# Kernel optimization log

Measured on AMD Instinct MI355X. Metric: run time of the kernel, lower is better.

The kernel has to match this reference:

```python
import jax, jax.numpy as jnp
import numpy as np

WIN = 9  # 9x9 local attention window

def conv2d(x, w, b=None, pad=1):
    # x: [B,C,H,W], w: [O,I,kh,kw]
    y = jax.lax.conv_general_dilated(x, w, (1, 1), [(pad, pad), (pad, pad)],
                                     dimension_numbers=('NCHW', 'OIHW', 'NCHW'))
    if b is not None:
        y = y + b[None, :, None, None]
    return y

def leaky(x):
    return jax.nn.leaky_relu(x, 0.2)

def local_similar(q, k):
    # TorchLocalAttention.f_similar: per-pixel dot(q[i,j], k[i+di-4, j+dj-4]) with zero pad,
    # kernel positions row-major (di*9+dj) -> output [B, 81, H, W]
    b, c, h, w = q.shape
    r = WIN // 2
    kp = jnp.pad(k, ((0, 0), (0, 0), (r, r), (r, r)))
    sims = []
    for di in range(WIN):
        for dj in range(WIN):
            sims.append(jnp.einsum('bchw,bchw->bhw', q, kp[:, :, di:di + h, dj:dj + w]))
    return jnp.stack(sims, axis=1)

def srp_forward(old, new, wq, bq, wk, bk, wv, bv, wo1, bo1, res_w1, res_w2, wo2, bo2):
    x = jnp.concatenate((old, new), axis=1)  # [B, C, H, W]
    att = local_similar(conv2d(x, wq, bq), conv2d(x, wk, bk))  # [B, 81, H, W]
    v = conv2d(att, wv, bv)  # [B, C, H, W]
    y = conv2d(x * v, wo1, bo1)
    n_res = res_w1.shape[0]
    for i in range(n_res):  # EBlock: ResBlocks (convs bias=False)
        h1 = leaky(conv2d(y, res_w1[i]))
        y = y + conv2d(h1, res_w2[i])
    y = conv2d(y, wo2, bo2)
    return y + x

def setup_inputs() -> dict:
    key = jax.random.key(0)
    B, Cn, Co, H, W = 4, 32, 32, 256, 256
    C = Cn + Co
    NRES = 8
    ks = jax.random.split(key, 16)
    s = 0.05
    inp = {
        'old': jax.random.normal(ks[0], (B, Co, H, W), jnp.float32),
        'new': jax.random.normal(ks[1], (B, Cn, H, W), jnp.float32),
        'wq': jax.random.normal(ks[2], (C, C, 3, 3), jnp.float32) * s,
        'bq': jax.random.normal(ks[3], (C,), jnp.float32) * s,
        'wk': jax.random.normal(ks[4], (C, C, 3, 3), jnp.float32) * s,
        'bk': jax.random.normal(ks[5], (C,), jnp.float32) * s,
        'wv': jax.random.normal(ks[6], (C, 81, 3, 3), jnp.float32) * s,
        'bv': jax.random.normal(ks[7], (C,), jnp.float32) * s,
        'wo1': jax.random.normal(ks[8], (C, C, 3, 3), jnp.float32) * s,
        'bo1': jax.random.normal(ks[9], (C,), jnp.float32) * s,
        'res_w1': jax.random.normal(ks[10], (NRES, C, C, 3, 3), jnp.float32) * s,
        'res_w2': jax.random.normal(ks[11], (NRES, C, C, 3, 3), jnp.float32) * s,
        'wo2': jax.random.normal(ks[12], (C, C, 3, 3), jnp.float32) * s,
        'bo2': jax.random.normal(ks[13], (C,), jnp.float32) * s,
    }
    return inp

def reference(old, new, wq, bq, wk, bk, wv, bv, wo1, bo1, res_w1, res_w2, wo2, bo2):
    return srp_forward(old, new, wq, bq, wk, bk, wv, bv, wo1, bo1, res_w1, res_w2, wo2, bo2)
```

## Files before the change

### kernel.cpp

```cpp
#include <hip/hip_runtime.h>
#include <hip/hip_bf16.h>


#define HH 256
#define WW 256
#define PLANE 65536

typedef _Float16 f16x8 __attribute__((ext_vector_type(8)));
typedef float    f32x4 __attribute__((ext_vector_type(4)));
typedef _Float16 h2    __attribute__((ext_vector_type(2)));

__device__ __forceinline__ unsigned short f2h(float f) {
    _Float16 h = (_Float16)f;
    return __builtin_bit_cast(unsigned short, h);
}
__device__ __forceinline__ float h2f(unsigned short u) {
    return (float)__builtin_bit_cast(_Float16, u);
}
__device__ __forceinline__ unsigned pack2h(float a, float b) {
    return (unsigned)f2h(a) | ((unsigned)f2h(b) << 16);
}
__device__ __forceinline__ float dot2h(unsigned a, unsigned b, float c) {
#if __has_builtin(__builtin_amdgcn_fdot2)
    return __builtin_amdgcn_fdot2(__builtin_bit_cast(h2, a),
                                  __builtin_bit_cast(h2, b), c, false);
#else
    h2 av = __builtin_bit_cast(h2, a), bv = __builtin_bit_cast(h2, b);
    return fmaf((float)av.x, (float)bv.x, fmaf((float)av.y, (float)bv.y, c));
#endif
}

__device__ __forceinline__ void gl16(const unsigned short* g, unsigned short* l) {
    __builtin_amdgcn_global_load_lds(
        (const __attribute__((address_space(1))) unsigned int*)(g),
        (__attribute__((address_space(3))) unsigned int*)(l),
        16, 0, 0);
}

template <int CIN, bool BIAS, bool LEAKY, bool ADDF, bool ADDX, bool MULX, bool OUTF, bool OUTB>
__global__ __launch_bounds__(256, 2) void conv_mfma(
    const unsigned short* __restrict__ in_pc,
    const unsigned short* __restrict__ wb,
    const float* __restrict__ bias,
    const unsigned short* __restrict__ addh,
    const unsigned short* __restrict__ xh,
    float* __restrict__ outf,
    unsigned short* __restrict__ outb)
{
    __shared__ unsigned short smem[28800];
    unsigned short* lds_in = smem;
    unsigned short* lds_w  = smem + 10368;

    const int tid = threadIdx.x;
    const int w   = tid >> 6;
    const int ln  = tid & 63;
    const int m   = ln & 15;
    const int q   = ln >> 4;
    const int b   = blockIdx.z;
    const int tx0 = blockIdx.x * 16, ty0 = blockIdx.y * 16;
    const size_t pixb = (size_t)b * PLANE;
    const bool interior = (blockIdx.x >= 1) && (blockIdx.x <= 14) &&
                          (blockIdx.y >= 1) && (blockIdx.y <= 14);

    f32x4 acc[4][4];
#pragma unroll
    for (int g = 0; g < 4; ++g)
#pragma unroll
        for (int p = 0; p < 4; ++p) acc[g][p] = (f32x4)0.f;

    for (int c2 = 0; c2 < CIN / 32; ++c2) {
        __syncthreads();
        if (interior) {
            const unsigned short* inb =
                in_pc + (pixb + (size_t)(ty0 - 1) * 256 + (tx0 - 1)) * CIN + c2 * 32;
#pragma unroll
            for (int it = 0; it < 5; ++it) {
                int u = it * 256 + tid;
                int pix = u >> 2, ps = u & 3;
                int part = ps ^ (pix & 3);
                int hy = pix / 18, hx = pix - hy * 18;
                gl16(inb + ((size_t)hy * 256 + hx) * CIN + part * 8,
                     &lds_in[(it * 256 + (tid & 192)) * 8]);
            }
            if (tid < 16) {
                int u = 1280 + tid;
                int pix = u >> 2, ps = u & 3;
                int part = ps ^ (pix & 3);
                int hy = pix / 18, hx = pix - hy * 18;
                gl16(inb + ((size_t)hy * 256 + hx) * CIN + part * 8,
                     &lds_in[1280 * 8]);
            }
        } else {
            for (int u = tid; u < 1296; u += 256) {
                int pix = u >> 2, part = u & 3;
                int hy = pix / 18, hx = pix - hy * 18;
                int gy = ty0 + hy - 1, gx = tx0 + hx - 1;
                uint4 val = make_uint4(0u, 0u, 0u, 0u);
                if ((unsigned)gy < 256u && (unsigned)gx < 256u)
                    val = *reinterpret_cast<const uint4*>(
                        in_pc + ((pixb + (size_t)gy * 256 + gx) * CIN + c2 * 32 + part * 8));
                *reinterpret_cast<uint4*>(&lds_in[pix * 32 + ((part ^ (pix & 3)) * 8)]) = val;
            }
        }
        {
            const int oc = tid >> 2, ps = tid & 3;
            const int part = ps ^ (oc & 3);
            const unsigned short* wsrc = wb + (size_t)oc * CIN + c2 * 32 + part * 8;
#pragma unroll
            for (int t = 0; t < 9; ++t)
                gl16(wsrc + (size_t)t * 64 * CIN,
                     &lds_w[t * 2048 + (tid & 192) * 8]);
        }
        __syncthreads();

#pragma unroll
        for (int t = 0; t < 9; ++t) {
            const int dy = t / 3, dx = t - dy * 3;
            f16x8 av[4], bv[4];
#pragma unroll
            for (int g = 0; g < 4; ++g) {
                int oc = g * 16 + m;
                av[g] = *reinterpret_cast<const f16x8*>(
                    &lds_w[t * 2048 + oc * 32 + ((q ^ (oc & 3)) * 8)]);
            }
#pragma unroll
            for (int p = 0; p < 4; ++p) {
                int hp = (w * 4 + p + dy) * 18 + m + dx;
                bv[p] = *reinterpret_cast<const f16x8*>(
                    &lds_in[hp * 32 + ((q ^ (hp & 3)) * 8)]);
            }
#pragma unroll
            for (int g = 0; g < 4; ++g)
#pragma unroll
                for (int p = 0; p < 4; ++p)
                    acc[g][p] = __builtin_amdgcn_mfma_f32_16x16x32_f16(
                        av[g], bv[p], acc[g][p], 0, 0, 0);
        }
    }

    const int colx = tx0 + m;
    float4 bvec[4];
    if (BIAS) {
#pragma unroll
        for (int g = 0; g < 4; ++g)
            bvec[g] = *reinterpret_cast<const float4*>(bias + g * 16 + q * 4);
    }
    if (OUTB) __syncthreads();

#pragma unroll
    for (int g = 0; g < 4; ++g) {
#pragma unroll
        for (int p = 0; p < 4; ++p) {
            const int prow = w * 4 + p;
            const int gy   = ty0 + prow;
            const size_t pixg = pixb + (size_t)gy * 256 + colx;
            const int oc0 = g * 16 + q * 4;
            ushort4 a4, x4;
            if (ADDF) a4 = *reinterpret_cast<const ushort4*>(addh + pixg * 64 + oc0);
            if (ADDX || MULX) x4 = *reinterpret_cast<const ushort4*>(xh + pixg * 64 + oc0);
            float vals[4];
#pragma unroll
            for (int r = 0; r < 4; ++r) {
                float v = acc[g][p][r];
                if (BIAS) v += reinterpret_cast<const float*>(&bvec[g])[r];
                if (LEAKY) v = (v >= 0.f) ? v : 0.2f * v;
                if (ADDF) v += h2f(reinterpret_cast<const unsigned short*>(&a4)[r]);
                if (ADDX) v += h2f(reinterpret_cast<const unsigned short*>(&x4)[r]);
                if (MULX) v *= h2f(reinterpret_cast<const unsigned short*>(&x4)[r]);
                if (OUTF)
                    outf[((size_t)(b * 64 + oc0 + r)) * PLANE + (size_t)gy * 256 + colx] = v;
                vals[r] = v;
            }
            if (OUTB) {
                ushort4 pk;
                pk.x = f2h(vals[0]); pk.y = f2h(vals[1]);
                pk.z = f2h(vals[2]); pk.w = f2h(vals[3]);
                int pix   = prow * 16 + m;
                int part8 = g * 4 + q;
                int p16   = (part8 >> 1) ^ (pix & 7);
                *reinterpret_cast<ushort4*>(&smem[pix * 64 + p16 * 8 + (part8 & 1) * 4]) = pk;
            }
        }
    }
    if (OUTB) {
        __syncthreads();
        for (int u = tid; u < 2048; u += 256) {
            int pix = u >> 3, p16 = u & 7;
            uint4 val = *reinterpret_cast<const uint4*>(
                &smem[pix * 64 + ((p16 ^ (pix & 7)) * 8)]);
            int gy = ty0 + (pix >> 4), gx = tx0 + (pix & 15);
            *reinterpret_cast<uint4*>(
                &outb[(pixb + (size_t)gy * 256 + gx) * 64 + p16 * 8]) = val;
        }
    }
}

__global__ __launch_bounds__(256)
void local_sim(
    const unsigned short* __restrict__ qh, const unsigned short* __restrict__ kh,
    unsigned short* __restrict__ att)
{
    __shared__ unsigned short lds_k[576 * 64];

    const int tid = threadIdx.x;
    const int tx = tid & 15, ty = tid >> 4;
    const int bx = blockIdx.x * 16, by = blockIdx.y * 16;
    const int b  = blockIdx.z;
    const size_t pixb = (size_t)b * PLANE;
    const bool interior = (blockIdx.x >= 1) && (blockIdx.x <= 14) &&
                          (blockIdx.y >= 1) && (blockIdx.y <= 14);

    if (interior) {
        const unsigned short* kb =
            kh + (pixb + (size_t)(by - 4) * 256 + (bx - 4)) * 64;
#pragma unroll
        for (int it = 0; it < 18; ++it) {
            int u = it * 256 + tid;
            int pix = u >> 3, sl = u & 7;
            int part = sl ^ ((pix ^ (pix >> 3)) & 7);
            int hy = pix / 24, hx = pix - hy * 24;
            gl16(kb + ((size_t)hy * 256 + hx) * 64 + part * 8,
                 &lds_k[(it * 256 + (tid & 192)) * 8]);
        }
    } else {
        for (int u = tid; u < 4608; u += 256) {
            int pix = u >> 3, part = u & 7;
            int hy = pix / 24, hx = pix - hy * 24;
            int gy = by + hy - 4, gx = bx + hx - 4;
            uint4 val = make_uint4(0u, 0u, 0u, 0u);
            if ((unsigned)gy < 256u && (unsigned)gx < 256u)
                val = *reinterpret_cast<const uint4*>(
                    kh + ((pixb + (size_t)gy * 256 + gx) * 64 + part * 8));
            int sl = part ^ ((pix ^ (pix >> 3)) & 7);
            *reinterpret_cast<uint4*>(&lds_k[pix * 64 + sl * 8]) = val;
        }
    }
    __syncthreads();

    const unsigned short* qbase = qh + (pixb + (size_t)(by + ty) * 256 + bx + tx) * 64;
    unsigned short* op = att + (pixb + (size_t)(by + ty) * 256 + bx + tx) * 96;

    uint4 qv[8];
#pragma unroll
    for (int j = 0; j < 8; ++j)
        qv[j] = *reinterpret_cast<const uint4*>(qbase + j * 8);

#pragma unroll
    for (int g = 0; g < 3; ++g) {
        float acc[27];
#pragma unroll
        for (int i = 0; i < 27; ++i) acc[i] = 0.f;

#pragma unroll
        for (int dil = 0; dil < 3; ++dil) {
            const int hrow = (ty + g * 3 + dil) * 24 + tx;
#pragma unroll
            for (int dj = 0; dj < 9; ++dj) {
                const int hp = hrow + dj;
                const int gs = (hp ^ (hp >> 3)) & 7;
                float s = acc[dil * 9 + dj];
#pragma unroll
                for (int part = 0; part < 8; ++part) {
                    const uint4 kv = *reinterpret_cast<const uint4*>(
                        &lds_k[hp * 64 + ((part ^ gs) * 8)]);
                    s = dot2h(qv[part].x, kv.x, s);
                    s = dot2h(qv[part].y, kv.y, s);
                    s = dot2h(qv[part].z, kv.z, s);
                    s = dot2h(qv[part].w, kv.w, s);
                }
                acc[dil * 9 + dj] = s;
            }
        }

        unsigned short* o = op + g * 27;
        if (g == 0) {
            uint4 A = {pack2h(acc[0], acc[1]),  pack2h(acc[2], acc[3]),
                       pack2h(acc[4], acc[5]),  pack2h(acc[6], acc[7])};
            uint4 B = {pack2h(acc[8], acc[9]),  pack2h(acc[10], acc[11]),
                       pack2h(acc[12], acc[13]), pack2h(acc[14], acc[15])};
            uint2 C = {pack2h(acc[16], acc[17]), pack2h(acc[18], acc[19])};
            uint2 D = {pack2h(acc[20], acc[21]), pack2h(acc[22], acc[23])};
            *reinterpret_cast<uint4*>(o)      = A;
            *reinterpret_cast<uint4*>(o + 8)  = B;
            *reinterpret_cast<uint2*>(o + 16) = C;
            *reinterpret_cast<uint2*>(o + 20) = D;
            *reinterpret_cast<unsigned*>(o + 24) = pack2h(acc[24], acc[25]);
            o[26] = f2h(acc[26]);
        } else if (g == 1) {
            o[0] = f2h(acc[0]);
            *reinterpret_cast<unsigned*>(o + 1) = pack2h(acc[1], acc[2]);
            *reinterpret_cast<unsigned*>(o + 3) = pack2h(acc[3], acc[4]);
            uint4 A = {pack2h(acc[5], acc[6]),   pack2h(acc[7], acc[8]),
                       pack2h(acc[9], acc[10]),  pack2h(acc[11], acc[12])};
            uint4 B = {pack2h(acc[13], acc[14]), pack2h(acc[15], acc[16]),
                       pack2h(acc[17], acc[18]), pack2h(acc[19], acc[20])};
            *reinterpret_cast<uint4*>(o + 5)  = A;
            *reinterpret_cast<uint4*>(o + 13) = B;
            uint2 C = {pack2h(acc[21], acc[22]), pack2h(acc[23], acc[24])};
            *reinterpret_cast<uint2*>(o + 21) = C;
            *reinterpret_cast<unsigned*>(o + 25) = pack2h(acc[25], acc[26]);
        } else {
            *reinterpret_cast<unsigned*>(o) = pack2h(acc[0], acc[1]);
            uint4 A = {pack2h(acc[2], acc[3]),   pack2h(acc[4], acc[5]),
                       pack2h(acc[6], acc[7]),   pack2h(acc[8], acc[9])};
            uint4 B = {pack2h(acc[10], acc[11]), pack2h(acc[12], acc[13]),
                       pack2h(acc[14], acc[15]), pack2h(acc[16], acc[17])};
            *reinterpret_cast<uint4*>(o + 2)  = A;
            *reinterpret_cast<uint4*>(o + 10) = B;
            uint2 C = {pack2h(acc[18], acc[19]), pack2h(acc[20], acc[21])};
            *reinterpret_cast<uint2*>(o + 18) = C;
            *reinterpret_cast<unsigned*>(o + 22) = pack2h(acc[22], acc[23]);
            *reinterpret_cast<unsigned*>(o + 24) = pack2h(acc[24], acc[25]);
            o[26] = f2h(acc[26]);
        }
    }

    op[81] = 0;
    *reinterpret_cast<unsigned*>(op + 82) = 0u;
    uint2 z2 = {0u, 0u};
    uint4 z4 = {0u, 0u, 0u, 0u};
    *reinterpret_cast<uint2*>(op + 84) = z2;
    *reinterpret_cast<uint4*>(op + 88) = z4;
}

__global__ __launch_bounds__(256) void pack_x(
    const float* __restrict__ old_, const float* __restrict__ new_,
    unsigned short* __restrict__ xb)
{
    __shared__ unsigned short lds[256 * 64];
    const int tid = threadIdx.x;
    const int b = blockIdx.y;
    const size_t pixbase = (size_t)blockIdx.x * 256;
#pragma unroll
    for (int cg = 0; cg < 8; ++cg) {
        unsigned pk[4];
#pragma unroll
        for (int h = 0; h < 4; ++h) {
            int c0 = cg * 8 + h * 2;
            const float* s0 = (c0 < 32) ? old_ : new_;
            const float* s1 = ((c0 + 1) < 32) ? old_ : new_;
            float f0 = s0[((size_t)b * 32 + (c0 & 31)) * PLANE + pixbase + tid];
            float f1 = s1[((size_t)b * 32 + ((c0 + 1) & 31)) * PLANE + pixbase + tid];
            pk[h] = pack2h(f0, f1);
        }
        int p16 = cg ^ (tid & 7);
        uint4 v; v.x = pk[0]; v.y = pk[1]; v.z = pk[2]; v.w = pk[3];
        *reinterpret_cast<uint4*>(&lds[tid * 64 + p16 * 8]) = v;
    }
    __syncthreads();
    for (int r = 0; r < 8; ++r) {
        int u = r * 256 + tid;
        int pix = u >> 3, p16 = u & 7;
        uint4 v = *reinterpret_cast<const uint4*>(&lds[pix * 64 + ((p16 ^ (pix & 7)) * 8)]);
        *reinterpret_cast<uint4*>(
            &xb[((size_t)b * PLANE + pixbase + pix) * 64 + p16 * 8]) = v;
    }
}

__global__ void prep_wstd(const float* __restrict__ wq, const float* __restrict__ wk,
                          const float* __restrict__ wo1, const float* __restrict__ wo2,
                          const float* __restrict__ rw1, const float* __restrict__ rw2,
                          unsigned short* __restrict__ wstd)
{
    const int c = blockIdx.y;
    const float* src;
    if (c == 0) src = wq;
    else if (c == 1) src = wk;
    else if (c == 2) src = wo1;
    else if (c == 3) src = wo2;
    else if (c < 12) src = rw1 + (size_t)(c - 4) * 36864;
    else src = rw2 + (size_t)(c - 12) * 36864;
    int idx = blockIdx.x * 256 + threadIdx.x;
    int o = idx >> 6, i = idx & 63;
    const float* s = src + (size_t)(o * 64 + i) * 9;
    unsigned short* d = wstd + (size_t)c * 36864 + (size_t)o * 64 + i;
#pragma unroll
    for (int t = 0; t < 9; ++t) d[(size_t)t * 4096] = f2h(s[t]);
}

__global__ void prep_wv(const float* __restrict__ wv, unsigned short* __restrict__ wv96)
{
    int idx = blockIdx.x * 256 + threadIdx.x;
    int o = idx / 96, i = idx - o * 96;
    unsigned short* d = wv96 + (size_t)o * 96 + i;
    if (i < 81) {
        const float* s = wv + (size_t)(o * 81 + i) * 9;
#pragma unroll
        for (int t = 0; t < 9; ++t) d[(size_t)t * 6144] = f2h(s[t]);
    } else {
#pragma unroll
        for (int t = 0; t < 9; ++t) d[(size_t)t * 6144] = 0;
    }
}

extern "C" void kernel_launch(void* const* d_in, const int* in_sizes, int n_in,
                              void* d_out, int out_size, void* d_ws, size_t ws_size,
                              hipStream_t stream)
{
    const float* old_ = (const float*)d_in[0];
    const float* new_ = (const float*)d_in[1];
    const float* wq  = (const float*)d_in[2];  const float* bq  = (const float*)d_in[3];
    const float* wk  = (const float*)d_in[4];  const float* bk  = (const float*)d_in[5];
    const float* wv  = (const float*)d_in[6];  const float* bv  = (const float*)d_in[7];
    const float* wo1 = (const float*)d_in[8];  const float* bo1 = (const float*)d_in[9];
    const float* rw1 = (const float*)d_in[10]; const float* rw2 = (const float*)d_in[11];
    const float* wo2 = (const float*)d_in[12]; const float* bo2 = (const float*)d_in[13];
    float* out = (float*)d_out;

    char* ws = (char*)d_ws;
    unsigned short* X   = (unsigned short*)(ws);
    unsigned short* P1  = (unsigned short*)(ws + 33554432ull);
    unsigned short* P2  = (unsigned short*)(ws + 67108864ull);
    unsigned short* P3  = (unsigned short*)(ws + 100663296ull);
    unsigned short* wst = (unsigned short*)(ws + 150994944ull);
    unsigned short* wv96= (unsigned short*)(ws + 152469504ull);

    const dim3 cgrid(16, 16, 4), cblk(256);

    prep_wstd<<<dim3(16, 20), 256, 0, stream>>>(wq, wk, wo1, wo2, rw1, rw2, wst);
    prep_wv<<<dim3(24), 256, 0, stream>>>(wv, wv96);
    pack_x<<<dim3(256, 4), 256, 0, stream>>>(old_, new_, X);

    conv_mfma<64, true, false, false, false, false, false, true>
        <<<cgrid, cblk, 0, stream>>>(X, wst + 0ull * 36864, bq, nullptr, nullptr, nullptr, P1);
    conv_mfma<64, true, false, false, false, false, false, true>
        <<<cgrid, cblk, 0, stream>>>(X, wst + 1ull * 36864, bk, nullptr, nullptr, nullptr, P2);
    local_sim<<<cgrid, cblk, 0, stream>>>(P1, P2, P3);
    conv_mfma<96, true, false, false, false, true, false, true>
        <<<cgrid, cblk, 0, stream>>>(P3, wv96, bv, nullptr, X, nullptr, P2);
    conv_mfma<64, true, false, false, false, false, false, true>
        <<<cgrid, cblk, 0, stream>>>(P2, wst + 2ull * 36864, bo1, nullptr, nullptr, nullptr, P1);
    for (int i = 0; i < 8; ++i) {
        unsigned short* ysrc = (i & 1) ? P3 : P1;
        unsigned short* ydst = (i & 1) ? P1 : P3;
        conv_mfma<64, false, true, false, false, false, false, true>
            <<<cgrid, cblk, 0, stream>>>(ysrc, wst + (size_t)(4 + i) * 36864, nullptr,
                                         nullptr, nullptr, nullptr, P2);
        conv_mfma<64, false, false, true, false, false, false, true>
            <<<cgrid, cblk, 0, stream>>>(P2, wst + (size_t)(12 + i) * 36864, nullptr,
                                         ysrc, nullptr, nullptr, ydst);
    }
    conv_mfma<64, true, false, false, true, false, true, false>
        <<<cgrid, cblk, 0, stream>>>(P1, wst + 3ull * 36864, bo2, nullptr, X, out, nullptr);
}
```

Measured before the change: 878.4 us.

## Double-buffer input tiles in LDS and read conv weights directly from global

```diff
diff --git a/kernel.cpp b/kernel.cpp
--- a/kernel.cpp
+++ b/kernel.cpp
@@ -47,9 +47,7 @@
     float* __restrict__ outf,
     unsigned short* __restrict__ outb)
 {
-    __shared__ unsigned short smem[28800];
-    unsigned short* lds_in = smem;
-    unsigned short* lds_w  = smem + 10368;
+    __shared__ unsigned short smem[20736];
 
     const int tid = threadIdx.x;
     const int w   = tid >> 6;
@@ -62,17 +60,10 @@
     const bool interior = (blockIdx.x >= 1) && (blockIdx.x <= 14) &&
                           (blockIdx.y >= 1) && (blockIdx.y <= 14);
 
-    f32x4 acc[4][4];
-#pragma unroll
-    for (int g = 0; g < 4; ++g)
-#pragma unroll
-        for (int p = 0; p < 4; ++p) acc[g][p] = (f32x4)0.f;
-
-    for (int c2 = 0; c2 < CIN / 32; ++c2) {
-        __syncthreads();
+    auto stage = [&](int c2s, unsigned short* dst) {
         if (interior) {
             const unsigned short* inb =
-                in_pc + (pixb + (size_t)(ty0 - 1) * 256 + (tx0 - 1)) * CIN + c2 * 32;
+                in_pc + (pixb + (size_t)(ty0 - 1) * 256 + (tx0 - 1)) * CIN + c2s * 32;
 #pragma unroll
             for (int it = 0; it < 5; ++it) {
                 int u = it * 256 + tid;
@@ -80,7 +71,7 @@
                 int part = ps ^ (pix & 3);
                 int hy = pix / 18, hx = pix - hy * 18;
                 gl16(inb + ((size_t)hy * 256 + hx) * CIN + part * 8,
-                     &lds_in[(it * 256 + (tid & 192)) * 8]);
+                     &dst[(it * 256 + (tid & 192)) * 8]);
             }
             if (tid < 16) {
                 int u = 1280 + tid;
@@ -88,7 +79,7 @@
                 int part = ps ^ (pix & 3);
                 int hy = pix / 18, hx = pix - hy * 18;
                 gl16(inb + ((size_t)hy * 256 + hx) * CIN + part * 8,
-                     &lds_in[1280 * 8]);
+                     &dst[1280 * 8]);
             }
         } else {
             for (int u = tid; u < 1296; u += 256) {
@@ -98,36 +89,42 @@
                 uint4 val = make_uint4(0u, 0u, 0u, 0u);
                 if ((unsigned)gy < 256u && (unsigned)gx < 256u)
                     val = *reinterpret_cast<const uint4*>(
-                        in_pc + ((pixb + (size_t)gy * 256 + gx) * CIN + c2 * 32 + part * 8));
-                *reinterpret_cast<uint4*>(&lds_in[pix * 32 + ((part ^ (pix & 3)) * 8)]) = val;
-            }
-        }
-        {
-            const int oc = tid >> 2, ps = tid & 3;
-            const int part = ps ^ (oc & 3);
-            const unsigned short* wsrc = wb + (size_t)oc * CIN + c2 * 32 + part * 8;
-#pragma unroll
-            for (int t = 0; t < 9; ++t)
-                gl16(wsrc + (size_t)t * 64 * CIN,
-                     &lds_w[t * 2048 + (tid & 192) * 8]);
-        }
-        __syncthreads();
+                        in_pc + ((pixb + (size_t)gy * 256 + gx) * CIN + c2s * 32 + part * 8));
+                *reinterpret_cast<uint4*>(&dst[pix * 32 + ((part ^ (pix & 3)) * 8)]) = val;
+            }
+        }
+    };
+
+    f32x4 acc[4][4];
+#pragma unroll
+    for (int g = 0; g < 4; ++g)
+#pragma unroll
+        for (int p = 0; p < 4; ++p) acc[g][p] = (f32x4)0.f;
+
+    constexpr int NC = CIN / 32;
+    const unsigned short* wlane = wb + q * 8;
+
+    stage(0, smem);
+    __syncthreads();
+
+    for (int c2 = 0; c2 < NC; ++c2) {
+        unsigned short* cbuf = (c2 & 1) ? smem + 10368 : smem;
+        if (c2 + 1 < NC)
+            stage(c2 + 1, ((c2 + 1) & 1) ? smem + 10368 : smem);
 
 #pragma unroll
         for (int t = 0; t < 9; ++t) {
             const int dy = t / 3, dx = t - dy * 3;
             f16x8 av[4], bv[4];
 #pragma unroll
-            for (int g = 0; g < 4; ++g) {
-                int oc = g * 16 + m;
+            for (int g = 0; g < 4; ++g)
                 av[g] = *reinterpret_cast<const f16x8*>(
-                    &lds_w[t * 2048 + oc * 32 + ((q ^ (oc & 3)) * 8)]);
-            }
+                    wlane + (size_t)(t * 64 + g * 16 + m) * CIN + c2 * 32);
 #pragma unroll
             for (int p = 0; p < 4; ++p) {
                 int hp = (w * 4 + p + dy) * 18 + m + dx;
                 bv[p] = *reinterpret_cast<const f16x8*>(
-                    &lds_in[hp * 32 + ((q ^ (hp & 3)) * 8)]);
+                    &cbuf[hp * 32 + ((q ^ (hp & 3)) * 8)]);
             }
 #pragma unroll
             for (int g = 0; g < 4; ++g)
@@ -136,6 +133,7 @@
                     acc[g][p] = __builtin_amdgcn_mfma_f32_16x16x32_f16(
                         av[g], bv[p], acc[g][p], 0, 0, 0);
         }
+        if (c2 + 1 < NC) __syncthreads();
     }
 
     const int colx = tx0 + m;
```

After: 1.267 ms. 44.2% more time.
